# Kernel optimization log

Hardware: AMD Instinct MI355X
Metric: run time of the kernel (lower is better)

The kernel has to match this reference:

```python
import jax, jax.numpy as jnp
import numpy as np

EMBED_DIM = 584  # module-global, used as softmax scale base (C ** -0.5)


def setup_inputs() -> dict:
    key = jax.random.key(0)
    ks = jax.random.split(key, 7)
    B, T, C, H, D = 16, 1024, 584, 8, 73
    x = jax.random.normal(ks[0], (B, T, C), dtype=jnp.float32)
    memory = jax.random.normal(ks[1], (B, T, C), dtype=jnp.float32)
    s = 0.02
    Wq = jax.random.normal(ks[2], (H, C, D), dtype=jnp.float32) * s
    Wk = jax.random.normal(ks[3], (H, C, D), dtype=jnp.float32) * s
    Wv = jax.random.normal(ks[4], (H, C, D), dtype=jnp.float32) * s
    Wp = jax.random.normal(ks[5], (C, C), dtype=jnp.float32) * s
    bp = jnp.zeros((C,), dtype=jnp.float32)
    return {"x": x, "memory": memory, "Wq": Wq, "Wk": Wk, "Wv": Wv, "Wp": Wp, "bp": bp}


def reference(x, memory, Wq, Wk, Wv, Wp, bp):
    B, T, C = x.shape
    # per-head projections, vectorized over heads: [B, H, T, D]
    q = jnp.einsum('btc,hcd->bhtd', x, Wq)
    k = jnp.einsum('bsc,hcd->bhsd', memory, Wk)
    v = jnp.einsum('btc,hcd->bhtd', x, Wv)  # NOTE: value from x, per original code
    # scale uses full embed dim C (not head size), per original code
    scores = jnp.einsum('bhtd,bhsd->bhts', q, k) * (C ** -0.5)
    weights = jax.nn.softmax(scores, axis=-1)
    # dropout is identity in eval/reference mode
    out = jnp.einsum('bhts,bhsd->bhtd', weights, v)  # requires S == T (matches original)
    out = out.transpose(0, 2, 1, 3).reshape(B, T, C)  # concat heads on last dim
    out = out @ Wp + bp  # output projection (dropout identity)
    return out
```

## Files before the change

kernel.cpp:

```cpp
#include <hip/hip_runtime.h>
#include <hip/hip_bf16.h>

typedef unsigned short u16;
typedef __attribute__((ext_vector_type(4))) unsigned short u16x4;
typedef __attribute__((ext_vector_type(8))) unsigned short u16x8;
typedef __attribute__((ext_vector_type(8))) __bf16 bf16x8;
typedef __attribute__((ext_vector_type(4))) float f32x4;

#define BB 16
#define TSEQ 1024
#define CC 584
#define HH 8
#define DHD 73
#define NR (BB*TSEQ)
#define KPW 640
#define DP 80
#define HD (HH*DP)
#define NP3 768
#define PPITCH 88
#define CEXP 0.0596985934f

__device__ __forceinline__ u16 f2bf(float f) {
  __bf16 h = (__bf16)f;
  return __builtin_bit_cast(u16, h);
}
__device__ __forceinline__ bf16x8 as_bf(u16x8 v) { return __builtin_bit_cast(bf16x8, v); }

#define GLL16(g, l) __builtin_amdgcn_global_load_lds( \
    (const __attribute__((address_space(1))) void*)(g), \
    (__attribute__((address_space(3))) void*)(l), 16, 0, 0)

#define BARRIER() asm volatile("s_barrier" ::: "memory")
#define VMW7()    asm volatile("s_waitcnt vmcnt(7)" ::: "memory")
#define VMW6()    asm volatile("s_waitcnt vmcnt(6)" ::: "memory")
#define VMW2()    asm volatile("s_waitcnt vmcnt(2)" ::: "memory")
#define VMW0()    asm volatile("s_waitcnt vmcnt(0)" ::: "memory")

#define PKA 10240
#define PKB2 600
#define PKC2 240
__global__ void pack_all_kernel(const float* __restrict__ x, const float* __restrict__ mem,
                                const float* __restrict__ Wq, const float* __restrict__ Wk,
                                const float* __restrict__ Wv, const float* __restrict__ Wp,
                                u16* __restrict__ xmb, u16* __restrict__ wt,
                                u16* __restrict__ wpt) {
  const int bidx = blockIdx.x;
  const int tid = threadIdx.x;
  if (bidx < PKA) {
    int idx = bidx * 256 + tid;
    int row = idx / (KPW / 8);
    int c8  = (idx % (KPW / 8)) * 8;
    u16x8 o = {0, 0, 0, 0, 0, 0, 0, 0};
    if (c8 < CC) {
      const float* src = (row < NR) ? &x[(size_t)row * CC + c8]
                                    : &mem[(size_t)(row - NR) * CC + c8];
      f32x4 a = *(const f32x4*)src;
      f32x4 b = *(const f32x4*)(src + 4);
#pragma unroll
      for (int t = 0; t < 4; t++) { o[t] = f2bf(a[t]); o[4 + t] = f2bf(b[t]); }
    }
    *(u16x8*)&xmb[(size_t)row * KPW + c8] = o;
  } else if (bidx < PKA + PKB2) {
    const int base = (bidx - PKA) * 2048 + tid;
#pragma unroll
    for (int e = 0; e < 8; e++) {
      int idx = base + e * 256;
      int w   = idx / (HD * KPW);
      int rem = idx % (HD * KPW);
      int n = rem / KPW;
      int k = rem % KPW;
      int h = n / DP, d = n % DP;
      u16 val = 0;
      if (d < DHD && k < CC) {
        const float* W = (w == 0) ? Wq : ((w == 1) ? Wv : Wk);
        val = f2bf(W[((size_t)h * CC + k) * DHD + d]);
      }
      wt[idx] = val;
    }
  } else {
    const int base = (bidx - PKA - PKB2) * 2048 + tid;
#pragma unroll
    for (int e = 0; e < 8; e++) {
      int idx = base + e * 256;
      int n = idx / KPW;
      int c = idx % KPW;
      u16 val = 0;
      if (n < CC && c < CC) val = f2bf(Wp[(size_t)c * CC + n]);
      wpt[idx] = val;
    }
  }
}


__device__ __forceinline__ void rd_a4(bf16x8 (&a)[4][2], const u16* lds, int base,
                                      int sw0, int sw1) {
#pragma unroll
  for (int mq = 0; mq < 4; mq++) {
    const int r = base + mq * 1024;
    a[mq][0] = as_bf(*(const u16x8*)&lds[r + sw0]);
    a[mq][1] = as_bf(*(const u16x8*)&lds[r + sw1]);
  }
}
template <int NQ>
__device__ __forceinline__ void rd_bn(bf16x8 (&b)[NQ][2], const u16* lds, int base,
                                      int sw0, int sw1) {
#pragma unroll
  for (int nq = 0; nq < NQ; nq++) {
    const int r = base + nq * 1024;
    b[nq][0] = as_bf(*(const u16x8*)&lds[r + sw0]);
    b[nq][1] = as_bf(*(const u16x8*)&lds[r + sw1]);
  }
}
__device__ __forceinline__ void s_a1(const u16* gA, u16* ldst, int t, int lb) {
  GLL16(gA + (size_t)128 * KPW + (size_t)t * 64, ldst + lb + 8192);
  GLL16(gA + (size_t)192 * KPW + (size_t)t * 64, ldst + lb + 12288);
}
template <int NB>
__device__ __forceinline__ void s_a0b(const u16* gA, const u16* gB, u16* ldst,
                                      int t, int lb) {
  GLL16(gA + (size_t)t * 64, ldst + lb);
  GLL16(gA + (size_t)64 * KPW + (size_t)t * 64, ldst + lb + 4096);
#pragma unroll
  for (int u = 0; u < NB; u++)
    GLL16(gB + (size_t)(u * 64) * KPW + (size_t)t * 64, ldst + lb + 16384 + u * 4096);
}
template <int NQ>
__device__ __forceinline__ void mm4n(f32x4 (&acc)[4][NQ], const bf16x8 (&a)[4][2],
                                     const bf16x8 (&b)[NQ][2]) {
  __builtin_amdgcn_s_setprio(1);
#pragma unroll
  for (int mq = 0; mq < 4; mq++)
#pragma unroll
    for (int nq = 0; nq < NQ; nq++) {
      f32x4 c = acc[mq][nq];
      c = __builtin_amdgcn_mfma_f32_16x16x32_bf16(a[mq][0], b[nq][0], c, 0, 0, 0);
      c = __builtin_amdgcn_mfma_f32_16x16x32_bf16(a[mq][1], b[nq][1], c, 0, 0, 0);
      acc[mq][nq] = c;
    }
  __builtin_amdgcn_s_setprio(0);
}

template <int MODE>
__global__ __launch_bounds__(512, 2) void gemm8_kernel(
    const u16* __restrict__ A, const u16* __restrict__ Bt,
    void* __restrict__ CoutV, void* __restrict__ CoutV2,
    const float* __restrict__ bias) {
  constexpr int NB = (MODE == 4) ? 2 : 3;
  constexpr int NQ = NB;
  constexpr int WN = NQ * 16;
  constexpr int SB = 16384 + NB * 4096;
  extern __shared__ u16 lds[];
  const int tid  = threadIdx.x;
  const int lane = tid & 63;
  const int q15  = lane & 15;
  const int quad = lane >> 4;
  const int wave = tid >> 6;
  const int wmi  = wave >> 2;
  const int wni  = wave & 3;

  const int cpx = gridDim.x >> 3;
  const int bid = (blockIdx.x & 7) * cpx + (blockIdx.x >> 3);

  int m0, n0, npart;
  if (MODE == 4) {
    if (bid < 640) {
      m0 = (bid / 10) * 256; int nt = bid % 10;
      if (nt < 5) { n0 = nt * 128; npart = 0; }
      else        { n0 = 640 + (nt - 5) * 128; npart = 1; }
    } else {
      int b2 = bid - 640;
      m0 = NR + (b2 / 5) * 256; n0 = 1280 + (b2 % 5) * 128; npart = 2;
    }
  } else {
    m0 = (bid >> 2) * 256; n0 = (bid & 3) * 192; npart = 0;
  }

  const int tr   = tid >> 3;
  const int scol = ((tid & 7) ^ (tr & 7)) * 8;
  const u16* gA = &A[(size_t)(m0 + tr) * KPW + scol];
  const u16* gB = &Bt[(size_t)(n0 + tr) * KPW + scol];
  u16* ldst = &lds[tid * 8];

  const int rb  = q15 & 7;
  const int sw0 = (quad ^ rb) * 8;
  const int sw1 = ((quad + 4) ^ rb) * 8;
  const int arow = (wmi * 64 + q15) * 64;
  const int brow = (wni * WN + q15) * 64;

  f32x4 acc[2][4][NQ];
#pragma unroll
  for (int i = 0; i < 2; i++)
#pragma unroll
    for (int j = 0; j < 4; j++)
#pragma unroll
      for (int k = 0; k < NQ; k++) acc[i][j][k] = (f32x4){0.f, 0.f, 0.f, 0.f};
  bf16x8 a[4][2], b[NQ][2];

  s_a0b<NB>(gA, gB, ldst, 0, 0);
  s_a1(gA, ldst, 0, 0);
  s_a0b<NB>(gA, gB, ldst, 1, SB);
  if constexpr (NB == 2) VMW6(); else VMW7();
  BARRIER();

#pragma unroll 1
  for (int t = 0; t < 10; ++t) {
    const int lb = (t & 1) * SB;
    const int lbo = lb ^ SB;
    rd_a4(a, lds, lb + arow, sw0, sw1);
    rd_bn<NQ>(b, lds, lb + 16384 + brow, sw0, sw1);
    if (t < 9) s_a1(gA, ldst, t + 1, lbo);
    if (t == 9) { VMW0(); } else { if constexpr (NB == 2) VMW6(); else VMW7(); }
    BARRIER();
    mm4n<NQ>(acc[0], a, b);
    BARRIER();
    rd_a4(a, lds, lb + 8192 + arow, sw0, sw1);
    if (t < 8) { s_a0b<NB>(gA, gB, ldst, t + 2, lb);
                 if constexpr (NB == 2) VMW6(); else VMW7(); }
    else if (t == 8) { VMW2(); }
    BARRIER();
    mm4n<NQ>(acc[1], a, b);
    BARRIER();
  }

  const int rowb = m0 + wmi * 64 + quad * 4;
  const int colb = n0 + wni * WN + q15;
#pragma unroll
  for (int mh = 0; mh < 2; mh++)
#pragma unroll
    for (int mq = 0; mq < 4; mq++)
#pragma unroll
      for (int nq = 0; nq < NQ; nq++) {
        const f32x4 av = acc[mh][mq][nq];
        const int row = rowb + mh * 128 + mq * 16;
        const int col = colb + nq * 16;
        if (MODE == 4) {
          if (npart == 2) {
            u16* Cout = (u16*)CoutV2;
            const int rk = row - NR;
            const int ck = col - 1280;
#pragma unroll
            for (int r = 0; r < 4; r++)
              Cout[(size_t)(rk + r) * HD + ck] = f2bf(av[r]);
          } else if (npart == 0) {
            u16* Cout = (u16*)CoutV;
#pragma unroll
            for (int r = 0; r < 4; r++)
              Cout[(size_t)(row + r) * HD + col] = f2bf(av[r]);
          } else {
            u16* Cout = (u16*)CoutV;
            const int vn = col - 640;
            const int bb = row >> 10;
            const int tl = row & 1023;
            u16x4 pk;
#pragma unroll
            for (int r = 0; r < 4; r++) pk[r] = f2bf(av[r]);
            *(u16x4*)&Cout[(size_t)(NR * HD) + ((size_t)(bb * HD + vn)) * TSEQ + tl] = pk;
          }
        } else {
          if (col < CC) {
            float* Cout = (float*)CoutV;
            const float bvv = bias[col];
#pragma unroll
            for (int r = 0; r < 4; r++)
              Cout[(size_t)(row + r) * CC + col] = av[r] + bvv;
          }
        }
      }
}

__global__ __launch_bounds__(256, 3) void attn_kernel(
    const u16* __restrict__ qb, const u16* __restrict__ kb,
    const u16* __restrict__ vt, u16* __restrict__ attn) {
  __shared__ u16 smem[11264 + 64 * 88 + 80 * 72];
  u16* Pt = smem;
  u16* Ks = smem + 11264;
  u16* Vs = smem + 11264 + 64 * 88;

  const int tid  = threadIdx.x;
  const int lane = tid & 63;
  const int wave = tid >> 6;
  const int q15  = lane & 15;
  const int quad = lane >> 4;
  const int bid  = blockIdx.x;
  const int loc  = bid >> 3;
  const int pair = (bid & 7) * 16 + (loc >> 3);
  const int b  = pair >> 3;
  const int h  = pair & 7;
  const int t0 = (loc & 7) * 128;
  const int wq0 = wave * 32;
  const bool w3 = (tid < 128);

  int krow[3], kc[3], vrow[3], vc[3];
#pragma unroll
  for (int p = 0; p < 3; p++) {
    int qk = tid + 256 * p;
    krow[p] = qk / 10; kc[p] = (qk % 10) * 8;
    vrow[p] = qk >> 3; vc[p] = (qk & 7) * 8;
  }
  const u16* kbase = &kb[(size_t)(b * TSEQ) * HD + h * DP];
  const u16* vbase = &vt[(size_t)(b * HD + h * DP) * TSEQ];

  bf16x8 aq[2][2], aqt[2];
  {
    const u16x8 z = {0, 0, 0, 0, 0, 0, 0, 0};
#pragma unroll
    for (int n = 0; n < 2; n++) {
      const size_t qrow = (size_t)(b * TSEQ + t0 + wq0 + n * 16 + q15) * HD + h * DP;
#pragma unroll
      for (int kcx = 0; kcx < 2; kcx++)
        aq[n][kcx] = as_bf(*(const u16x8*)&qb[qrow + kcx * 32 + quad * 8]);
      u16x8 tload = z;
      if (quad < 2) tload = *(const u16x8*)&qb[qrow + 64 + quad * 8];
      aqt[n] = as_bf(tload);
    }
  }

  if (tid < 128) {
    const u16x8 z = {0, 0, 0, 0, 0, 0, 0, 0};
    size_t base = (size_t)(b * TSEQ + t0 + tid) * KPW + CC;
#pragma unroll
    for (int c = 0; c < (KPW - CC) / 8; c++) *(u16x8*)&attn[base + c * 8] = z;
  }

  float lsum[2] = {0.f, 0.f};
  f32x4 oacc[2][5];
#pragma unroll
  for (int m = 0; m < 2; m++)
#pragma unroll
    for (int jd = 0; jd < 5; jd++) oacc[m][jd] = (f32x4){0.f, 0.f, 0.f, 0.f};

  u16* Ptw = &Pt[wave * 32 * PPITCH];

  u16x8 kreg[3], vreg[3];
#pragma unroll
  for (int p = 0; p < 2; p++) {
    kreg[p] = *(const u16x8*)&kbase[(size_t)krow[p] * HD + kc[p]];
    vreg[p] = *(const u16x8*)&vbase[(size_t)vrow[p] * TSEQ + vc[p]];
  }
  if (w3) {
    kreg[2] = *(const u16x8*)&kbase[(size_t)krow[2] * HD + kc[2]];
    vreg[2] = *(const u16x8*)&vbase[(size_t)vrow[2] * TSEQ + vc[2]];
  }

  for (int si = 0; si < 16; ++si) {
#pragma unroll
    for (int p = 0; p < 2; p++) {
      *(u16x8*)&Ks[krow[p] * 88 + kc[p]] = kreg[p];
      *(u16x8*)&Vs[vrow[p] * 72 + vc[p]] = vreg[p];
    }
    if (w3) {
      *(u16x8*)&Ks[krow[2] * 88 + kc[2]] = kreg[2];
      *(u16x8*)&Vs[vrow[2] * 72 + vc[2]] = vreg[2];
    }
    __syncthreads();

    if (si < 15) {
      const int s1 = (si + 1) * 64;
#pragma unroll
      for (int p = 0; p < 2; p++) {
        kreg[p] = *(const u16x8*)&kbase[(size_t)(s1 + krow[p]) * HD + kc[p]];
        vreg[p] = *(const u16x8*)&vbase[(size_t)vrow[p] * TSEQ + s1 + vc[p]];
      }
      if (w3) {
        kreg[2] = *(const u16x8*)&kbase[(size_t)(s1 + krow[2]) * HD + kc[2]];
        vreg[2] = *(const u16x8*)&vbase[(size_t)vrow[2] * TSEQ + s1 + vc[2]];
      }
    }

    f32x4 st[4][2];
#pragma unroll
    for (int mt = 0; mt < 4; mt++)
#pragma unroll
      for (int n = 0; n < 2; n++) st[mt][n] = (f32x4){0.f, 0.f, 0.f, 0.f};
#pragma unroll
    for (int kcx = 0; kcx < 2; kcx++) {
      bf16x8 ak[4];
#pragma unroll
      for (int mt = 0; mt < 4; mt++)
        ak[mt] = as_bf(*(const u16x8*)&Ks[(mt * 16 + q15) * 88 + kcx * 32 + quad * 8]);
#pragma unroll
      for (int mt = 0; mt < 4; mt++)
#pragma unroll
        for (int n = 0; n < 2; n++)
          st[mt][n] = __builtin_amdgcn_mfma_f32_16x16x32_bf16(ak[mt], aq[n][kcx], st[mt][n], 0, 0, 0);
    }
    {
      const u16x8 z = {0, 0, 0, 0, 0, 0, 0, 0};
#pragma unroll
      for (int mt = 0; mt < 4; mt++) {
        u16x8 tl = z;
        if (quad < 2) tl = *(const u16x8*)&Ks[(mt * 16 + q15) * 88 + 64 + quad * 8];
        bf16x8 akt = as_bf(tl);
#pragma unroll
        for (int n = 0; n < 2; n++)
          st[mt][n] = __builtin_amdgcn_mfma_f32_16x16x32_bf16(akt, aqt[n], st[mt][n], 0, 0, 0);
      }
    }

#pragma unroll
    for (int mt = 0; mt < 4; mt++)
#pragma unroll
      for (int n = 0; n < 2; n++) {
        f32x4 pv;
#pragma unroll
        for (int r = 0; r < 4; r++) pv[r] = __builtin_amdgcn_exp2f(st[mt][n][r] * CEXP);
        lsum[n] += (pv[0] + pv[1]) + (pv[2] + pv[3]);
        u16x4 pk;
#pragma unroll
        for (int r = 0; r < 4; r++) pk[r] = f2bf(pv[r]);
        *(u16x4*)&Ptw[(n * 16 + q15) * PPITCH + mt * 16 + quad * 4] = pk;
      }

#pragma unroll
    for (int kcx = 0; kcx < 2; kcx++) {
      bf16x8 ap[2];
#pragma unroll
      for (int m = 0; m < 2; m++)
        ap[m] = as_bf(*(const u16x8*)&Ptw[(m * 16 + q15) * PPITCH + kcx * 32 + quad * 8]);
#pragma unroll
      for (int jd = 0; jd < 5; jd++) {
        bf16x8 bv = as_bf(*(const u16x8*)&Vs[(jd * 16 + q15) * 72 + kcx * 32 + quad * 8]);
#pragma unroll
        for (int m = 0; m < 2; m++)
          oacc[m][jd] = __builtin_amdgcn_mfma_f32_16x16x32_bf16(ap[m], bv, oacc[m][jd], 0, 0, 0);
      }
    }
    __syncthreads();
  }

  float lr[2];
#pragma unroll
  for (int n = 0; n < 2; n++) {
    float s = lsum[n];
    s += __shfl_xor(s, 16);
    s += __shfl_xor(s, 32);
    lr[n] = s;
  }

#pragma unroll
  for (int m = 0; m < 2; m++) {
#pragma unroll
    for (int r = 0; r < 4; r++) {
      const float inv = 1.f / __shfl(lr[m], quad * 4 + r);
      const int trow = t0 + wq0 + m * 16 + quad * 4 + r;
#pragma unroll
      for (int jd = 0; jd < 5; jd++) {
        const int d = jd * 16 + q15;
        if (d < DHD)
          attn[(size_t)(b * TSEQ + trow) * KPW + h * DHD + d] = f2bf(oacc[m][jd][r] * inv);
      }
    }
  }
}


extern "C" void kernel_launch(void* const* d_in, const int* in_sizes, int n_in,
                              void* d_out, int out_size, void* d_ws, size_t ws_size,
                              hipStream_t stream) {
  const float* x   = (const float*)d_in[0];
  const float* mem = (const float*)d_in[1];
  const float* Wq  = (const float*)d_in[2];
  const float* Wk  = (const float*)d_in[3];
  const float* Wv  = (const float*)d_in[4];
  const float* Wp  = (const float*)d_in[5];
  const float* bp  = (const float*)d_in[6];
  float* out = (float*)d_out;

  char* ws = (char*)d_ws;
  const size_t SZ_XMB = (size_t)2 * NR * KPW * 2;
  const size_t SZ_WT  = (size_t)3 * HD * KPW * 2;
  const size_t SZ_WPT = (size_t)NP3 * KPW * 2;
  const size_t SZ_QB  = (size_t)NR * HD * 2;

  u16* xmb    = (u16*)(ws);
  u16* attn_o = (u16*)(ws);
  u16* wt     = (u16*)(ws + SZ_XMB);
  u16* wp_t   = (u16*)(ws + SZ_XMB + SZ_WT);
  u16* q_buf  = (u16*)(ws + SZ_XMB + SZ_WT + SZ_WPT);
  u16* vt_buf = q_buf + (size_t)NR * HD;
  u16* k_buf  = (u16*)(ws + SZ_XMB + SZ_WT + SZ_WPT + 2 * SZ_QB);

  (void)in_sizes; (void)n_in; (void)out_size; (void)ws_size;

  static bool s_attr = false;
  if (!s_attr) {
    (void)hipFuncSetAttribute((const void*)gemm8_kernel<4>,
                              hipFuncAttributeMaxDynamicSharedMemorySize, 114688);
    (void)hipFuncSetAttribute((const void*)gemm8_kernel<2>,
                              hipFuncAttributeMaxDynamicSharedMemorySize, 114688);
    s_attr = true;
  }

  pack_all_kernel<<<PKA + PKB2 + PKC2, 256, 0, stream>>>(x, mem, Wq, Wk, Wv, Wp,
                                                         xmb, wt, wp_t);

  gemm8_kernel<4><<<960, 512, 98304, stream>>>(xmb, wt, q_buf, k_buf, nullptr);

  attn_kernel<<<BB * HH * (TSEQ / 128), 256, 0, stream>>>(q_buf, k_buf, vt_buf, attn_o);

  gemm8_kernel<2><<<256, 512, 114688, stream>>>(attn_o, wp_t, out, nullptr, bp);
}
```

Baseline: 286.9 us.

## Double attention query tile per block and batch pack work per thread

The attention kernel now uses 512 threads (8 waves) per block, each block covering 256 query rows instead of 128. Each staged K/V tile is therefore shared by twice as many queries, which halves K/V global reloads and block count, and the P staging buffer moves to dynamic shared memory. Separately, the activation pack stage now has each thread convert eight 8-element chunks instead of one, cutting the block count for that stage by 8x. The trade-off is larger LDS per block, fewer resident blocks per CU and fewer blocks overall, which may lower occupancy and load balance.

```diff
diff --git a/kernel.cpp b/kernel.cpp
--- a/kernel.cpp
+++ b/kernel.cpp
@@ -36,7 +36,7 @@
 #define VMW2()    asm volatile("s_waitcnt vmcnt(2)" ::: "memory")
 #define VMW0()    asm volatile("s_waitcnt vmcnt(0)" ::: "memory")
 
-#define PKA 10240
+#define PKA2 1280
 #define PKB2 600
 #define PKC2 240
 __global__ void pack_all_kernel(const float* __restrict__ x, const float* __restrict__ mem,
@@ -46,22 +46,26 @@
                                 u16* __restrict__ wpt) {
   const int bidx = blockIdx.x;
   const int tid = threadIdx.x;
-  if (bidx < PKA) {
-    int idx = bidx * 256 + tid;
-    int row = idx / (KPW / 8);
-    int c8  = (idx % (KPW / 8)) * 8;
-    u16x8 o = {0, 0, 0, 0, 0, 0, 0, 0};
-    if (c8 < CC) {
-      const float* src = (row < NR) ? &x[(size_t)row * CC + c8]
-                                    : &mem[(size_t)(row - NR) * CC + c8];
-      f32x4 a = *(const f32x4*)src;
-      f32x4 b = *(const f32x4*)(src + 4);
-#pragma unroll
-      for (int t = 0; t < 4; t++) { o[t] = f2bf(a[t]); o[4 + t] = f2bf(b[t]); }
-    }
-    *(u16x8*)&xmb[(size_t)row * KPW + c8] = o;
-  } else if (bidx < PKA + PKB2) {
-    const int base = (bidx - PKA) * 2048 + tid;
+  if (bidx < PKA2) {
+    const int base = bidx * 2048 + tid;
+#pragma unroll
+    for (int e = 0; e < 8; e++) {
+      int idx = base + e * 256;
+      int row = idx / (KPW / 8);
+      int c8  = (idx % (KPW / 8)) * 8;
+      u16x8 o = {0, 0, 0, 0, 0, 0, 0, 0};
+      if (c8 < CC) {
+        const float* src = (row < NR) ? &x[(size_t)row * CC + c8]
+                                      : &mem[(size_t)(row - NR) * CC + c8];
+        f32x4 a = *(const f32x4*)src;
+        f32x4 b = *(const f32x4*)(src + 4);
+#pragma unroll
+        for (int t = 0; t < 4; t++) { o[t] = f2bf(a[t]); o[4 + t] = f2bf(b[t]); }
+      }
+      *(u16x8*)&xmb[(size_t)row * KPW + c8] = o;
+    }
+  } else if (bidx < PKA2 + PKB2) {
+    const int base = (bidx - PKA2) * 2048 + tid;
 #pragma unroll
     for (int e = 0; e < 8; e++) {
       int idx = base + e * 256;
@@ -78,7 +82,7 @@
       wt[idx] = val;
     }
   } else {
-    const int base = (bidx - PKA - PKB2) * 2048 + tid;
+    const int base = (bidx - PKA2 - PKB2) * 2048 + tid;
 #pragma unroll
     for (int e = 0; e < 8; e++) {
       int idx = base + e * 256;
@@ -268,13 +272,13 @@
       }
 }
 
-__global__ __launch_bounds__(256, 3) void attn_kernel(
+__global__ __launch_bounds__(512, 2) void attn_kernel(
     const u16* __restrict__ qb, const u16* __restrict__ kb,
     const u16* __restrict__ vt, u16* __restrict__ attn) {
-  __shared__ u16 smem[11264 + 64 * 88 + 80 * 72];
-  u16* Pt = smem;
-  u16* Ks = smem + 11264;
-  u16* Vs = smem + 11264 + 64 * 88;
+  extern __shared__ u16 alds[];
+  u16* Pt = alds;
+  u16* Ks = alds + 8 * 32 * PPITCH;
+  u16* Vs = Ks + 64 * 88;
 
   const int tid  = threadIdx.x;
   const int lane = tid & 63;
@@ -283,20 +287,17 @@
   const int quad = lane >> 4;
   const int bid  = blockIdx.x;
   const int loc  = bid >> 3;
-  const int pair = (bid & 7) * 16 + (loc >> 3);
+  const int pair = (bid & 7) * 16 + (loc >> 2);
   const int b  = pair >> 3;
   const int h  = pair & 7;
-  const int t0 = (loc & 7) * 128;
+  const int t0 = (loc & 3) * 256;
   const int wq0 = wave * 32;
-  const bool w3 = (tid < 128);
-
-  int krow[3], kc[3], vrow[3], vc[3];
-#pragma unroll
-  for (int p = 0; p < 3; p++) {
-    int qk = tid + 256 * p;
-    krow[p] = qk / 10; kc[p] = (qk % 10) * 8;
-    vrow[p] = qk >> 3; vc[p] = (qk & 7) * 8;
-  }
+  const bool p1 = (tid < 128);
+
+  const int k0r = tid / 10,          k0c = (tid % 10) * 8;
+  const int k1r = (512 + tid) / 10,  k1c = ((512 + tid) % 10) * 8;
+  const int v0r = tid >> 3,          v0c = (tid & 7) * 8;
+  const int v1r = 64 + (tid >> 3),   v1c = v0c;
   const u16* kbase = &kb[(size_t)(b * TSEQ) * HD + h * DP];
   const u16* vbase = &vt[(size_t)(b * HD + h * DP) * TSEQ];
 
@@ -315,7 +316,7 @@
     }
   }
 
-  if (tid < 128) {
+  if (tid < 256) {
     const u16x8 z = {0, 0, 0, 0, 0, 0, 0, 0};
     size_t base = (size_t)(b * TSEQ + t0 + tid) * KPW + CC;
 #pragma unroll
@@ -331,39 +332,30 @@
 
   u16* Ptw = &Pt[wave * 32 * PPITCH];
 
-  u16x8 kreg[3], vreg[3];
-#pragma unroll
-  for (int p = 0; p < 2; p++) {
-    kreg[p] = *(const u16x8*)&kbase[(size_t)krow[p] * HD + kc[p]];
-    vreg[p] = *(const u16x8*)&vbase[(size_t)vrow[p] * TSEQ + vc[p]];
-  }
-  if (w3) {
-    kreg[2] = *(const u16x8*)&kbase[(size_t)krow[2] * HD + kc[2]];
-    vreg[2] = *(const u16x8*)&vbase[(size_t)vrow[2] * TSEQ + vc[2]];
+  u16x8 kreg0, kreg1, vreg0, vreg1;
+  kreg0 = *(const u16x8*)&kbase[(size_t)k0r * HD + k0c];
+  vreg0 = *(const u16x8*)&vbase[(size_t)v0r * TSEQ + v0c];
+  if (p1) {
+    kreg1 = *(const u16x8*)&kbase[(size_t)k1r * HD + k1c];
+    vreg1 = *(const u16x8*)&vbase[(size_t)v1r * TSEQ + v1c];
   }
 
   for (int si = 0; si < 16; ++si) {
-#pragma unroll
-    for (int p = 0; p < 2; p++) {
-      *(u16x8*)&Ks[krow[p] * 88 + kc[p]] = kreg[p];
-      *(u16x8*)&Vs[vrow[p] * 72 + vc[p]] = vreg[p];
-    }
-    if (w3) {
-      *(u16x8*)&Ks[krow[2] * 88 + kc[2]] = kreg[2];
-      *(u16x8*)&Vs[vrow[2] * 72 + vc[2]] = vreg[2];
+    *(u16x8*)&Ks[k0r * 88 + k0c] = kreg0;
+    *(u16x8*)&Vs[v0r * 72 + v0c] = vreg0;
+    if (p1) {
+      *(u16x8*)&Ks[k1r * 88 + k1c] = kreg1;
+      *(u16x8*)&Vs[v1r * 72 + v1c] = vreg1;
     }
     __syncthreads();
 
     if (si < 15) {
       const int s1 = (si + 1) * 64;
-#pragma unroll
-      for (int p = 0; p < 2; p++) {
-        kreg[p] = *(const u16x8*)&kbase[(size_t)(s1 + krow[p]) * HD + kc[p]];
-        vreg[p] = *(const u16x8*)&vbase[(size_t)vrow[p] * TSEQ + s1 + vc[p]];
-      }
-      if (w3) {
-        kreg[2] = *(const u16x8*)&kbase[(size_t)(s1 + krow[2]) * HD + kc[2]];
-        vreg[2] = *(const u16x8*)&vbase[(size_t)vrow[2] * TSEQ + s1 + vc[2]];
+      kreg0 = *(const u16x8*)&kbase[(size_t)(s1 + k0r) * HD + k0c];
+      vreg0 = *(const u16x8*)&vbase[(size_t)v0r * TSEQ + s1 + v0c];
+      if (p1) {
+        kreg1 = *(const u16x8*)&kbase[(size_t)(s1 + k1r) * HD + k1c];
+        vreg1 = *(const u16x8*)&vbase[(size_t)v1r * TSEQ + s1 + v1c];
       }
     }
 
@@ -488,15 +480,17 @@
                               hipFuncAttributeMaxDynamicSharedMemorySize, 114688);
     (void)hipFuncSetAttribute((const void*)gemm8_kernel<2>,
                               hipFuncAttributeMaxDynamicSharedMemorySize, 114688);
+    (void)hipFuncSetAttribute((const void*)attn_kernel,
+                              hipFuncAttributeMaxDynamicSharedMemorySize, 67840);
     s_attr = true;
   }
 
-  pack_all_kernel<<<PKA + PKB2 + PKC2, 256, 0, stream>>>(x, mem, Wq, Wk, Wv, Wp,
-                                                         xmb, wt, wp_t);
+  pack_all_kernel<<<PKA2 + PKB2 + PKC2, 256, 0, stream>>>(x, mem, Wq, Wk, Wv, Wp,
+                                                          xmb, wt, wp_t);
 
   gemm8_kernel<4><<<960, 512, 98304, stream>>>(xmb, wt, q_buf, k_buf, nullptr);
 
-  attn_kernel<<<BB * HH * (TSEQ / 128), 256, 0, stream>>>(q_buf, k_buf, vt_buf, attn_o);
+  attn_kernel<<<BB * HH * (TSEQ / 256), 512, 67840, stream>>>(q_buf, k_buf, vt_buf, attn_o);
 
   gemm8_kernel<2><<<256, 512, 114688, stream>>>(attn_o, wp_t, out, nullptr, bp);
 }
```

After: 285.7 us. Within noise of the previous version (-0.4%).

## Switch GEMMs to 128x128 tiles with 4 waves and simpler double-buffered staging

Applied to the files above, without the earlier changes.

Replaces the 256-row, 8-wave GEMM tiling (split into two M halves per K step) with a 128x128 tile computed by 4 waves of 64x64 each. It uses a simple two-stage LDS double buffer that loads A and B in one staging call per K step. Grid sizes grow, to 1920 blocks for the QKV projection and 768 for the output projection, and LDS per block drops to 64 KiB. The pack kernel also processes 8 elements per thread for the activation conversion, which cuts its block count. The tradeoff is more blocks and less reuse per block, in exchange for more resident blocks and fewer barriers per tile.

```diff
diff --git a/kernel.cpp b/kernel.cpp
--- a/kernel.cpp
+++ b/kernel.cpp
@@ -31,12 +31,10 @@
     (__attribute__((address_space(3))) void*)(l), 16, 0, 0)
 
 #define BARRIER() asm volatile("s_barrier" ::: "memory")
-#define VMW7()    asm volatile("s_waitcnt vmcnt(7)" ::: "memory")
-#define VMW6()    asm volatile("s_waitcnt vmcnt(6)" ::: "memory")
-#define VMW2()    asm volatile("s_waitcnt vmcnt(2)" ::: "memory")
+#define VMW8()    asm volatile("s_waitcnt vmcnt(8)" ::: "memory")
 #define VMW0()    asm volatile("s_waitcnt vmcnt(0)" ::: "memory")
 
-#define PKA 10240
+#define PKA2 1280
 #define PKB2 600
 #define PKC2 240
 __global__ void pack_all_kernel(const float* __restrict__ x, const float* __restrict__ mem,
@@ -46,22 +44,26 @@
                                 u16* __restrict__ wpt) {
   const int bidx = blockIdx.x;
   const int tid = threadIdx.x;
-  if (bidx < PKA) {
-    int idx = bidx * 256 + tid;
-    int row = idx / (KPW / 8);
-    int c8  = (idx % (KPW / 8)) * 8;
-    u16x8 o = {0, 0, 0, 0, 0, 0, 0, 0};
-    if (c8 < CC) {
-      const float* src = (row < NR) ? &x[(size_t)row * CC + c8]
-                                    : &mem[(size_t)(row - NR) * CC + c8];
-      f32x4 a = *(const f32x4*)src;
-      f32x4 b = *(const f32x4*)(src + 4);
-#pragma unroll
-      for (int t = 0; t < 4; t++) { o[t] = f2bf(a[t]); o[4 + t] = f2bf(b[t]); }
-    }
-    *(u16x8*)&xmb[(size_t)row * KPW + c8] = o;
-  } else if (bidx < PKA + PKB2) {
-    const int base = (bidx - PKA) * 2048 + tid;
+  if (bidx < PKA2) {
+    const int base = bidx * 2048 + tid;
+#pragma unroll
+    for (int e = 0; e < 8; e++) {
+      int idx = base + e * 256;
+      int row = idx / (KPW / 8);
+      int c8  = (idx % (KPW / 8)) * 8;
+      u16x8 o = {0, 0, 0, 0, 0, 0, 0, 0};
+      if (c8 < CC) {
+        const float* src = (row < NR) ? &x[(size_t)row * CC + c8]
+                                      : &mem[(size_t)(row - NR) * CC + c8];
+        f32x4 a = *(const f32x4*)src;
+        f32x4 b = *(const f32x4*)(src + 4);
+#pragma unroll
+        for (int t = 0; t < 4; t++) { o[t] = f2bf(a[t]); o[4 + t] = f2bf(b[t]); }
+      }
+      *(u16x8*)&xmb[(size_t)row * KPW + c8] = o;
+    }
+  } else if (bidx < PKA2 + PKB2) {
+    const int base = (bidx - PKA2) * 2048 + tid;
 #pragma unroll
     for (int e = 0; e < 8; e++) {
       int idx = base + e * 256;
@@ -78,7 +80,7 @@
       wt[idx] = val;
     }
   } else {
-    const int base = (bidx - PKA - PKB2) * 2048 + tid;
+    const int base = (bidx - PKA2 - PKB2) * 2048 + tid;
 #pragma unroll
     for (int e = 0; e < 8; e++) {
       int idx = base + e * 256;
@@ -92,87 +94,55 @@
 }
 
 
-__device__ __forceinline__ void rd_a4(bf16x8 (&a)[4][2], const u16* lds, int base,
-                                      int sw0, int sw1) {
-#pragma unroll
-  for (int mq = 0; mq < 4; mq++) {
-    const int r = base + mq * 1024;
-    a[mq][0] = as_bf(*(const u16x8*)&lds[r + sw0]);
-    a[mq][1] = as_bf(*(const u16x8*)&lds[r + sw1]);
-  }
-}
-template <int NQ>
-__device__ __forceinline__ void rd_bn(bf16x8 (&b)[NQ][2], const u16* lds, int base,
-                                      int sw0, int sw1) {
-#pragma unroll
-  for (int nq = 0; nq < NQ; nq++) {
-    const int r = base + nq * 1024;
-    b[nq][0] = as_bf(*(const u16x8*)&lds[r + sw0]);
-    b[nq][1] = as_bf(*(const u16x8*)&lds[r + sw1]);
-  }
-}
-__device__ __forceinline__ void s_a1(const u16* gA, u16* ldst, int t, int lb) {
-  GLL16(gA + (size_t)128 * KPW + (size_t)t * 64, ldst + lb + 8192);
-  GLL16(gA + (size_t)192 * KPW + (size_t)t * 64, ldst + lb + 12288);
-}
-template <int NB>
-__device__ __forceinline__ void s_a0b(const u16* gA, const u16* gB, u16* ldst,
-                                      int t, int lb) {
-  GLL16(gA + (size_t)t * 64, ldst + lb);
-  GLL16(gA + (size_t)64 * KPW + (size_t)t * 64, ldst + lb + 4096);
-#pragma unroll
-  for (int u = 0; u < NB; u++)
-    GLL16(gB + (size_t)(u * 64) * KPW + (size_t)t * 64, ldst + lb + 16384 + u * 4096);
-}
-template <int NQ>
-__device__ __forceinline__ void mm4n(f32x4 (&acc)[4][NQ], const bf16x8 (&a)[4][2],
-                                     const bf16x8 (&b)[NQ][2]) {
-  __builtin_amdgcn_s_setprio(1);
-#pragma unroll
-  for (int mq = 0; mq < 4; mq++)
-#pragma unroll
-    for (int nq = 0; nq < NQ; nq++) {
-      f32x4 c = acc[mq][nq];
-      c = __builtin_amdgcn_mfma_f32_16x16x32_bf16(a[mq][0], b[nq][0], c, 0, 0, 0);
-      c = __builtin_amdgcn_mfma_f32_16x16x32_bf16(a[mq][1], b[nq][1], c, 0, 0, 0);
-      acc[mq][nq] = c;
-    }
-  __builtin_amdgcn_s_setprio(0);
+__device__ __forceinline__ void rd4(bf16x8 (&v)[4][2], const u16* lds, int base,
+                                    int sw0, int sw1) {
+#pragma unroll
+  for (int q = 0; q < 4; q++) {
+    const int r = base + q * 1024;
+    v[q][0] = as_bf(*(const u16x8*)&lds[r + sw0]);
+    v[q][1] = as_bf(*(const u16x8*)&lds[r + sw1]);
+  }
+}
+__device__ __forceinline__ void stg128(const u16* gA, const u16* gB, u16* ldst, int t) {
+  const int lb = (t & 1) * 8192;
+  const size_t ko = (size_t)t * 64;
+#pragma unroll
+  for (int u = 0; u < 4; u++)
+    GLL16(gA + (size_t)(u * 32) * KPW + ko, ldst + lb + u * 2048);
+#pragma unroll
+  for (int u = 0; u < 4; u++)
+    GLL16(gB + (size_t)(u * 32) * KPW + ko, ldst + 16384 + lb + u * 2048);
 }
 
 template <int MODE>
-__global__ __launch_bounds__(512, 2) void gemm8_kernel(
+__global__ __launch_bounds__(256, 2) void gemm8_kernel(
     const u16* __restrict__ A, const u16* __restrict__ Bt,
     void* __restrict__ CoutV, void* __restrict__ CoutV2,
     const float* __restrict__ bias) {
-  constexpr int NB = (MODE == 4) ? 2 : 3;
-  constexpr int NQ = NB;
-  constexpr int WN = NQ * 16;
-  constexpr int SB = 16384 + NB * 4096;
   extern __shared__ u16 lds[];
   const int tid  = threadIdx.x;
   const int lane = tid & 63;
   const int q15  = lane & 15;
   const int quad = lane >> 4;
   const int wave = tid >> 6;
-  const int wmi  = wave >> 2;
-  const int wni  = wave & 3;
+  const int wmi  = wave >> 1;
+  const int wni  = wave & 1;
 
   const int cpx = gridDim.x >> 3;
   const int bid = (blockIdx.x & 7) * cpx + (blockIdx.x >> 3);
 
   int m0, n0, npart;
   if (MODE == 4) {
-    if (bid < 640) {
-      m0 = (bid / 10) * 256; int nt = bid % 10;
+    if (bid < 1280) {
+      m0 = (bid / 10) * 128; int nt = bid % 10;
       if (nt < 5) { n0 = nt * 128; npart = 0; }
       else        { n0 = 640 + (nt - 5) * 128; npart = 1; }
     } else {
-      int b2 = bid - 640;
-      m0 = NR + (b2 / 5) * 256; n0 = 1280 + (b2 % 5) * 128; npart = 2;
+      int b2 = bid - 1280;
+      m0 = NR + (b2 / 5) * 128; n0 = 1280 + (b2 % 5) * 128; npart = 2;
     }
   } else {
-    m0 = (bid >> 2) * 256; n0 = (bid & 3) * 192; npart = 0;
+    m0 = (bid / 6) * 128; n0 = (bid % 6) * 128; npart = 0;
   }
 
   const int tr   = tid >> 3;
@@ -185,87 +155,84 @@
   const int sw0 = (quad ^ rb) * 8;
   const int sw1 = ((quad + 4) ^ rb) * 8;
   const int arow = (wmi * 64 + q15) * 64;
-  const int brow = (wni * WN + q15) * 64;
-
-  f32x4 acc[2][4][NQ];
-#pragma unroll
-  for (int i = 0; i < 2; i++)
-#pragma unroll
-    for (int j = 0; j < 4; j++)
-#pragma unroll
-      for (int k = 0; k < NQ; k++) acc[i][j][k] = (f32x4){0.f, 0.f, 0.f, 0.f};
-  bf16x8 a[4][2], b[NQ][2];
-
-  s_a0b<NB>(gA, gB, ldst, 0, 0);
-  s_a1(gA, ldst, 0, 0);
-  s_a0b<NB>(gA, gB, ldst, 1, SB);
-  if constexpr (NB == 2) VMW6(); else VMW7();
-  BARRIER();
+  const int brow = (wni * 64 + q15) * 64;
+
+  f32x4 acc[4][4];
+#pragma unroll
+  for (int i = 0; i < 4; i++)
+#pragma unroll
+    for (int j = 0; j < 4; j++) acc[i][j] = (f32x4){0.f, 0.f, 0.f, 0.f};
+
+  stg128(gA, gB, ldst, 0);
+  stg128(gA, gB, ldst, 1);
+  VMW8(); BARRIER();
 
 #pragma unroll 1
   for (int t = 0; t < 10; ++t) {
-    const int lb = (t & 1) * SB;
-    const int lbo = lb ^ SB;
-    rd_a4(a, lds, lb + arow, sw0, sw1);
-    rd_bn<NQ>(b, lds, lb + 16384 + brow, sw0, sw1);
-    if (t < 9) s_a1(gA, ldst, t + 1, lbo);
-    if (t == 9) { VMW0(); } else { if constexpr (NB == 2) VMW6(); else VMW7(); }
+    const int lb = (t & 1) * 8192;
+    bf16x8 a[4][2], b[4][2];
+    rd4(a, lds, lb + arow, sw0, sw1);
+    rd4(b, lds, 16384 + lb + brow, sw0, sw1);
+    __builtin_amdgcn_s_setprio(1);
+#pragma unroll
+    for (int mq = 0; mq < 4; mq++)
+#pragma unroll
+      for (int nq = 0; nq < 4; nq++) {
+        f32x4 c = acc[mq][nq];
+        c = __builtin_amdgcn_mfma_f32_16x16x32_bf16(a[mq][0], b[nq][0], c, 0, 0, 0);
+        c = __builtin_amdgcn_mfma_f32_16x16x32_bf16(a[mq][1], b[nq][1], c, 0, 0, 0);
+        acc[mq][nq] = c;
+      }
+    __builtin_amdgcn_s_setprio(0);
+    if (t == 9) break;
     BARRIER();
-    mm4n<NQ>(acc[0], a, b);
+    if (t < 8) { stg128(gA, gB, ldst, t + 2); VMW8(); }
+    else       { VMW0(); }
     BARRIER();
-    rd_a4(a, lds, lb + 8192 + arow, sw0, sw1);
-    if (t < 8) { s_a0b<NB>(gA, gB, ldst, t + 2, lb);
-                 if constexpr (NB == 2) VMW6(); else VMW7(); }
-    else if (t == 8) { VMW2(); }
-    BARRIER();
-    mm4n<NQ>(acc[1], a, b);
-    BARRIER();
   }
 
   const int rowb = m0 + wmi * 64 + quad * 4;
-  const int colb = n0 + wni * WN + q15;
-#pragma unroll
-  for (int mh = 0; mh < 2; mh++)
-#pragma unroll
-    for (int mq = 0; mq < 4; mq++)
-#pragma unroll
-      for (int nq = 0; nq < NQ; nq++) {
-        const f32x4 av = acc[mh][mq][nq];
-        const int row = rowb + mh * 128 + mq * 16;
-        const int col = colb + nq * 16;
-        if (MODE == 4) {
-          if (npart == 2) {
-            u16* Cout = (u16*)CoutV2;
-            const int rk = row - NR;
-            const int ck = col - 1280;
-#pragma unroll
-            for (int r = 0; r < 4; r++)
-              Cout[(size_t)(rk + r) * HD + ck] = f2bf(av[r]);
-          } else if (npart == 0) {
-            u16* Cout = (u16*)CoutV;
-#pragma unroll
-            for (int r = 0; r < 4; r++)
-              Cout[(size_t)(row + r) * HD + col] = f2bf(av[r]);
-          } else {
-            u16* Cout = (u16*)CoutV;
-            const int vn = col - 640;
-            const int bb = row >> 10;
-            const int tl = row & 1023;
-            u16x4 pk;
-#pragma unroll
-            for (int r = 0; r < 4; r++) pk[r] = f2bf(av[r]);
-            *(u16x4*)&Cout[(size_t)(NR * HD) + ((size_t)(bb * HD + vn)) * TSEQ + tl] = pk;
-          }
+  const int colb = n0 + wni * 64 + q15;
+#pragma unroll
+  for (int mq = 0; mq < 4; mq++)
+#pragma unroll
+    for (int nq = 0; nq < 4; nq++) {
+      const f32x4 av = acc[mq][nq];
+      const int row = rowb + mq * 16;
+      const int col = colb + nq * 16;
+      if (MODE == 4) {
+        if (npart == 2) {
+          u16* Cout = (u16*)CoutV2;
+          const int rk = row - NR;
+          const int ck = col - 1280;
+#pragma unroll
+          for (int r = 0; r < 4; r++)
+            Cout[(size_t)(rk + r) * HD + ck] = f2bf(av[r]);
+        } else if (npart == 0) {
+          u16* Cout = (u16*)CoutV;
+#pragma unroll
+          for (int r = 0; r < 4; r++)
+            Cout[(size_t)(row + r) * HD + col] = f2bf(av[r]);
         } else {
-          if (col < CC) {
-            float* Cout = (float*)CoutV;
-            const float bvv = bias[col];
-#pragma unroll
-            for (int r = 0; r < 4; r++)
-              Cout[(size_t)(row + r) * CC + col] = av[r] + bvv;
-          }
+          u16* Cout = (u16*)CoutV;
+          const int vn = col - 640;
+          const int bb = row >> 10;
+          const int tl = row & 1023;
+          u16x4 pk;
+#pragma unroll
+          for (int r = 0; r < 4; r++) pk[r] = f2bf(av[r]);
+          *(u16x4*)&Cout[(size_t)(NR * HD) + ((size_t)(bb * HD + vn)) * TSEQ + tl] = pk;
         }
-      }
+      } else {
+        if (col < CC) {
+          float* Cout = (float*)CoutV;
+          const float bvv = bias[col];
+#pragma unroll
+          for (int r = 0; r < 4; r++)
+            Cout[(size_t)(row + r) * CC + col] = av[r] + bvv;
+        }
+      }
+    }
 }
 
 __global__ __launch_bounds__(256, 3) void attn_kernel(
@@ -485,18 +452,18 @@
   static bool s_attr = false;
   if (!s_attr) {
     (void)hipFuncSetAttribute((const void*)gemm8_kernel<4>,
-                              hipFuncAttributeMaxDynamicSharedMemorySize, 114688);
+                              hipFuncAttributeMaxDynamicSharedMemorySize, 65536);
     (void)hipFuncSetAttribute((const void*)gemm8_kernel<2>,
-                              hipFuncAttributeMaxDynamicSharedMemorySize, 114688);
+                              hipFuncAttributeMaxDynamicSharedMemorySize, 65536);
     s_attr = true;
   }
 
-  pack_all_kernel<<<PKA + PKB2 + PKC2, 256, 0, stream>>>(x, mem, Wq, Wk, Wv, Wp,
-                                                         xmb, wt, wp_t);
-
-  gemm8_kernel<4><<<960, 512, 98304, stream>>>(xmb, wt, q_buf, k_buf, nullptr);
+  pack_all_kernel<<<PKA2 + PKB2 + PKC2, 256, 0, stream>>>(x, mem, Wq, Wk, Wv, Wp,
+                                                          xmb, wt, wp_t);
+
+  gemm8_kernel<4><<<1920, 256, 65536, stream>>>(xmb, wt, q_buf, k_buf, nullptr);
 
   attn_kernel<<<BB * HH * (TSEQ / 128), 256, 0, stream>>>(q_buf, k_buf, vt_buf, attn_o);
 
-  gemm8_kernel<2><<<256, 512, 114688, stream>>>(attn_o, wp_t, out, nullptr, bp);
-}
+  gemm8_kernel<2><<<768, 256, 65536, stream>>>(attn_o, wp_t, out, nullptr, bp);
+}
```

Measured after the change: 276.5 us, median of 2. -3.6%, faster.
